# Kernel optimization log

Measured on AMD Instinct MI355X. Metric: run time of the kernel, lower is better.

## Reference

```python
import jax, jax.numpy as jnp
import numpy as np
from jax import lax

TAU = 2.0
NUM_HEADS = 8
EPS = 1e-5
ALPHA = 4.0  # surrogate sigmoid sharpness

@jax.custom_vjp
def heaviside(x):
    # torch.heaviside(x, 1.0): 1 for x >= 0 (value 1 at x==0), 0 for x < 0
    return (x >= 0).astype(x.dtype)

def _hv_fwd(x):
    return (x >= 0).astype(x.dtype), x

def _hv_bwd(x, g):
    s = jax.nn.sigmoid(x * ALPHA)
    return (g * s * (1.0 - s) * ALPHA,)

heaviside.defvjp(_hv_fwd, _hv_bwd)

def lif(x):
    # Leaky-integrate-fire recurrence over leading time axis. x: [T, ...]
    def step(v, xt):
        v = v + (xt - v) / TAU                 # leakage
        s = heaviside(v - 1.0)                 # fire (v_threshold = 1.0)
        v = (1.0 - lax.stop_gradient(s)) * v   # hard reset (detached spike)
        return v, s
    _, spikes = lax.scan(step, jnp.zeros_like(x[0]), x)
    return spikes

def conv1x1(x, w):
    # x: [T,B,Cin,H,W], w: [Cout,Cin] (1x1 conv, no bias)
    return jnp.einsum('tbchw,dc->tbdhw', x, w)

def bn(x, gamma, beta, mean, var):
    # BatchNorm2d in eval mode (running stats), per-channel over axis 2
    shp = (1, 1, -1, 1, 1)
    inv = gamma.reshape(shp) / jnp.sqrt(var.reshape(shp) + EPS)
    return (x - mean.reshape(shp)) * inv + beta.reshape(shp)

def setup_inputs():
    key = jax.random.key(0)
    ks = jax.random.split(key, 10)
    T, B, C, H, W = 4, 32, 256, 16, 16
    Cv = C  # lamda_ratio = 1

    def w_init(k, o, i):
        return jax.random.normal(k, (o, i), jnp.float32) * (1.0 / np.sqrt(i))

    def bn_params(k, c):
        k1, k2, k3, k4 = jax.random.split(k, 4)
        gamma = jax.random.uniform(k1, (c,), jnp.float32, 0.5, 1.5)
        beta = jax.random.normal(k2, (c,), jnp.float32) * 0.1
        mean = jax.random.normal(k3, (c,), jnp.float32) * 0.1
        var = jax.random.uniform(k4, (c,), jnp.float32, 0.5, 1.5)
        return gamma, beta, mean, var

    x = jax.random.normal(ks[0], (T, B, C, H, W), jnp.float32)
    q_w = w_init(ks[1], C, C)
    k_w = w_init(ks[2], C, C)
    v_w = w_init(ks[3], Cv, C)
    proj_w = w_init(ks[4], C, Cv)
    q_gamma, q_beta, q_mean, q_var = bn_params(ks[5], C)
    k_gamma, k_beta, k_mean, k_var = bn_params(ks[6], C)
    v_gamma, v_beta, v_mean, v_var = bn_params(ks[7], Cv)
    p_gamma, p_beta, p_mean, p_var = bn_params(ks[8], C)
    return {
        'x': x,
        'q_w': q_w, 'q_gamma': q_gamma, 'q_beta': q_beta, 'q_mean': q_mean, 'q_var': q_var,
        'k_w': k_w, 'k_gamma': k_gamma, 'k_beta': k_beta, 'k_mean': k_mean, 'k_var': k_var,
        'v_w': v_w, 'v_gamma': v_gamma, 'v_beta': v_beta, 'v_mean': v_mean, 'v_var': v_var,
        'proj_w': proj_w, 'p_gamma': p_gamma, 'p_beta': p_beta, 'p_mean': p_mean, 'p_var': p_var,
    }

def reference(x, q_w, q_gamma, q_beta, q_mean, q_var,
              k_w, k_gamma, k_beta, k_mean, k_var,
              v_w, v_gamma, v_beta, v_mean, v_var,
              proj_w, p_gamma, p_beta, p_mean, p_var):
    T, B, C, H, W = x.shape
    N = H * W
    Cv = v_w.shape[0]
    hd = C // NUM_HEADS
    hdv = Cv // NUM_HEADS
    scale = (C // NUM_HEADS) ** -0.5

    xs = lif(x)  # head_spike

    q = lif(bn(conv1x1(xs, q_w), q_gamma, q_beta, q_mean, q_var))  # [T,B,C,H,W] binary
    k = lif(bn(conv1x1(xs, k_w), k_gamma, k_beta, k_mean, k_var))
    v = lif(bn(conv1x1(xs, v_w), v_gamma, v_beta, v_mean, v_var))  # [T,B,Cv,H,W]

    # channel c = h*hd + d; flatten spatial -> tokens N, split heads
    q = q.reshape(T, B, NUM_HEADS, hd, N).transpose(0, 1, 2, 4, 3)   # [T,B,h,N,d]
    k = k.reshape(T, B, NUM_HEADS, hd, N).transpose(0, 1, 2, 4, 3)
    v = v.reshape(T, B, NUM_HEADS, hdv, N).transpose(0, 1, 2, 4, 3)  # [T,B,h,N,dv]

    attn = jnp.einsum('tbhnd,tbhmd->tbhnm', q, k)                    # QK^T
    out = jnp.einsum('tbhnm,tbhmd->tbhnd', attn, v) * (scale * 2.0)  # (QK^T)V * 2*scale

    out = out.transpose(0, 1, 2, 4, 3).reshape(T, B, Cv, N)          # [T,B,Cv,N]
    out = lif(out)                                                   # attn_spike
    out = out.reshape(T, B, Cv, H, W)
    out = bn(conv1x1(out, proj_w), p_gamma, p_beta, p_mean, p_var)   # [T,B,C,H,W]
    return out
```

## Files before the change

kernel.cpp:

```cpp
#include <hip/hip_runtime.h>

#define TT 4
#define BB 32
#define CC 256
#define NN 256
#define EPSf 1e-5f
#define MULTf 0.35355339059327373f
#define MARGINf 1e-3f
#define FLAG_CAP 524288u

typedef __attribute__((ext_vector_type(8))) short s16x8;
typedef __attribute__((ext_vector_type(4))) float f32x4;
typedef unsigned char uchar;
typedef unsigned int uint;
typedef unsigned short ushort;

__device__ __forceinline__ ushort f2bf_rn(float f) {
  uint u = __float_as_uint(f);
  u = (u + 0x7FFFu + ((u >> 16) & 1u)) >> 16;
  return (ushort)u;
}
__device__ __forceinline__ float bf2f(ushort b) {
  return __uint_as_float(((uint)b) << 16);
}

__device__ __forceinline__ void gload_lds16(const void* g, void* l) {
  __builtin_amdgcn_global_load_lds(
      (const __attribute__((address_space(1))) uint*)g,
      (__attribute__((address_space(3))) uint*)l, 16, 0, 0);
}

__global__ __launch_bounds__(256) void k_lif_frag(const float* __restrict__ x,
                                                  uchar* __restrict__ xsF,
                                                  uchar* __restrict__ xsP) {
#pragma clang fp contract(off)
  const int tid = threadIdx.x;
  const int nt = blockIdx.x;
  const int ks = blockIdx.y;
  const int b = blockIdx.z;
  const int nl = tid & 63;
  const int oct = tid >> 6;
  const int n = nt * 64 + nl;
  const int c0 = ks * 32 + oct * 8;
  const size_t stride = (size_t)BB * CC * NN;
  const float* xb = x + ((size_t)b * CC + c0) * NN + n;

  float v[8];
#pragma unroll
  for (int j = 0; j < 8; ++j) v[j] = 0.f;

#pragma unroll
  for (int t = 0; t < TT; ++t) {
    ushort sp[8];
    uint pm = 0;
#pragma unroll
    for (int j = 0; j < 8; ++j) {
      float xt = xb[t * stride + (size_t)j * NN];
      float d = (xt - v[j]) * 0.5f;
      v[j] = v[j] + d;
      bool s = (v[j] >= 1.0f);
      sp[j] = s ? (ushort)0x3F80 : (ushort)0;
      if (s) { v[j] = 0.f; pm |= 1u << j; }
    }
    uint4* dst = reinterpret_cast<uint4*>(xsF) +
                 (((size_t)(t * BB + b) * 16 + (n >> 4)) * 512 + ks * 64 + oct * 16 + (n & 15));
    uint4 o;
    o.x = (uint)sp[0] | ((uint)sp[1] << 16);
    o.y = (uint)sp[2] | ((uint)sp[3] << 16);
    o.z = (uint)sp[4] | ((uint)sp[5] << 16);
    o.w = (uint)sp[6] | ((uint)sp[7] << 16);
    *dst = o;
    xsP[(((size_t)(t * BB + b) * NN + n) << 5) + ks * 4 + oct] = (uchar)pm;
  }
}

__global__ __launch_bounds__(256) void k_prep_w(
    const float* __restrict__ qw, const float* __restrict__ kw,
    const float* __restrict__ vw, const float* __restrict__ pw,
    uchar* __restrict__ wfq, uchar* __restrict__ wfp) {
  const int gid = blockIdx.x * 256 + threadIdx.x;
  const int ob2 = gid >> 9;
  const int e = gid & 511;
  const int ks = e >> 6, l = e & 63;
  const float* W;
  uchar* outb;
  int ob_out, nob;
  if (ob2 < 48) {
    const int sel = ob2 >> 4;
    W = sel == 0 ? qw : (sel == 1 ? kw : vw);
    W += ((size_t)((ob2 & 15) * 16 + (l & 15))) * CC;
    outb = wfq; ob_out = ob2; nob = 48;
  } else {
    W = pw + ((size_t)((ob2 - 48) * 16 + (l & 15))) * CC;
    outb = wfp; ob_out = ob2 - 48; nob = 16;
  }
  const int c0 = ks * 32 + (l >> 4) * 8;
  float wv[8];
  *reinterpret_cast<float4*>(&wv[0]) = *reinterpret_cast<const float4*>(W + c0);
  *reinterpret_cast<float4*>(&wv[4]) = *reinterpret_cast<const float4*>(W + c0 + 4);
  ushort hi[8], lo[8];
#pragma unroll
  for (int j = 0; j < 8; ++j) {
    hi[j] = f2bf_rn(wv[j]);
    lo[j] = f2bf_rn(wv[j] - bf2f(hi[j]));
  }
  const size_t base = (((size_t)ob_out * 8 + ks) * 64 + l) * 16;
  const size_t sstr = (size_t)nob * 8 * 64 * 16;
  *reinterpret_cast<uint4*>(outb + base) = *reinterpret_cast<const uint4*>(hi);
  *reinterpret_cast<uint4*>(outb + sstr + base) = *reinterpret_cast<const uint4*>(lo);
}

__global__ __launch_bounds__(256, 2) void k_qkv_mfma(
    const uchar* __restrict__ xsF, const uchar* __restrict__ wfq,
    const float* __restrict__ qga, const float* __restrict__ qbe, const float* __restrict__ qme, const float* __restrict__ qva,
    const float* __restrict__ kga, const float* __restrict__ kbe, const float* __restrict__ kme, const float* __restrict__ kva,
    const float* __restrict__ vga, const float* __restrict__ vbe, const float* __restrict__ vme, const float* __restrict__ vva,
    ushort* __restrict__ qp, uint* __restrict__ flags) {
  __shared__ short lsB[4][8][64][8];
  const int tid = threadIdx.x;
  const int w = tid >> 6, lane = tid & 63;
  const int lhi = lane >> 4, llo = lane & 15;
  const int wr = w >> 1, wc = w & 1;
  const int oc0 = blockIdx.x * 64;
  const int ntile = blockIdx.y;
  const int b = blockIdx.z;
  const int sel = oc0 >> 8;
  const float* G  = sel == 0 ? qga : (sel == 1 ? kga : vga);
  const float* Be = sel == 0 ? qbe : (sel == 1 ? kbe : vbe);
  const float* Mn = sel == 0 ? qme : (sel == 1 ? kme : vme);
  const float* Vr = sel == 0 ? qva : (sel == 1 ? kva : vva);

  s16x8 wfr[2][2][8];
#pragma unroll
  for (int s = 0; s < 2; ++s)
#pragma unroll
    for (int mf = 0; mf < 2; ++mf) {
      const int ob = blockIdx.x * 4 + wr * 2 + mf;
#pragma unroll
      for (int ks = 0; ks < 8; ++ks)
        wfr[s][mf][ks] = *reinterpret_cast<const s16x8*>(
            wfq + ((((size_t)s * 48 + ob) * 8 + ks) * 64 + lane) * 16);
    }

  float inv8[2][4], mean8[2][4], beta8[2][4];
#pragma unroll
  for (int mf = 0; mf < 2; ++mf)
#pragma unroll
    for (int r = 0; r < 4; ++r) {
      const int ocb = (oc0 & 255) + wr * 32 + mf * 16 + lhi * 4 + r;
      inv8[mf][r] = G[ocb] / sqrtf(Vr[ocb] + EPSf);
      mean8[mf][r] = Mn[ocb];
      beta8[mf][r] = Be[ocb];
    }

  float vst[2][2][4];
#pragma unroll
  for (int mf = 0; mf < 2; ++mf)
#pragma unroll
    for (int nf = 0; nf < 2; ++nf)
#pragma unroll
      for (int r = 0; r < 4; ++r) vst[mf][nf][r] = 0.f;
  uint fl = 0;

  for (int t = 0; t < TT; ++t) {
    __syncthreads();
    const uchar* src = xsF + (((size_t)(t * BB + b) * 16 + ntile * 4) * 8192);
#pragma unroll
    for (int k2 = 0; k2 < 8; ++k2) {
      const int chunk = w * 8 + k2;
      gload_lds16(src + (size_t)chunk * 1024 + lane * 16,
                  reinterpret_cast<char*>(&lsB[0][0][0][0]) + chunk * 1024);
    }
    __syncthreads();

    f32x4 acc[2][2];
#pragma unroll
    for (int mf = 0; mf < 2; ++mf)
#pragma unroll
      for (int nf = 0; nf < 2; ++nf) acc[mf][nf] = (f32x4){0.f, 0.f, 0.f, 0.f};

#pragma unroll
    for (int ks = 0; ks < 8; ++ks) {
      s16x8 b0 = *reinterpret_cast<const s16x8*>(&lsB[wc * 2][ks][lane][0]);
      s16x8 b1 = *reinterpret_cast<const s16x8*>(&lsB[wc * 2 + 1][ks][lane][0]);
#pragma unroll
      for (int s = 0; s < 2; ++s)
#pragma unroll
        for (int mf = 0; mf < 2; ++mf) {
          acc[mf][0] = __builtin_amdgcn_mfma_f32_16x16x32_bf16(wfr[s][mf][ks], b0, acc[mf][0], 0, 0, 0);
          acc[mf][1] = __builtin_amdgcn_mfma_f32_16x16x32_bf16(wfr[s][mf][ks], b1, acc[mf][1], 0, 0, 0);
        }
    }

    ushort* qrow = qp + (size_t)(t * BB + b) * 768 * 16;
#pragma unroll
    for (int mf = 0; mf < 2; ++mf)
#pragma unroll
      for (int nf = 0; nf < 2; ++nf)
#pragma unroll
        for (int r = 0; r < 4; ++r) {
          float y = (acc[mf][nf][r] - mean8[mf][r]) * inv8[mf][r] + beta8[mf][r];
          float v = vst[mf][nf][r];
          v = v + (y - v) * 0.5f;
          const bool sp = (v >= 1.0f);
          if (fabsf(v - 1.0f) < MARGINf) fl |= 1u << ((mf * 2 + nf) * 4 + r);
          const unsigned long long m = __ballot(sp);
          if (llo == r) {
            const int oc = oc0 + wr * 32 + mf * 16 + lhi * 4 + r;
            const int nw = ntile * 4 + wc * 2 + nf;
            qrow[(size_t)oc * 16 + nw] = (ushort)((m >> (lhi * 16)) & 0xFFFFull);
          }
          vst[mf][nf][r] = sp ? 0.f : v;
        }
  }

  if (fl) {
    const int cnt = __popc(fl);
    uint base = atomicAdd(flags, (uint)cnt);
#pragma unroll
    for (int mf = 0; mf < 2; ++mf)
#pragma unroll
      for (int nf = 0; nf < 2; ++nf)
#pragma unroll
        for (int r = 0; r < 4; ++r)
          if (fl & (1u << ((mf * 2 + nf) * 4 + r))) {
            const int oc = oc0 + wr * 32 + mf * 16 + lhi * 4 + r;
            const int n = ntile * 64 + wc * 32 + nf * 16 + llo;
            if (base < FLAG_CAP) flags[4 + base] = (((uint)(b << 10) | (uint)oc) << 8) | (uint)n;
            base++;
          }
  }
}

__global__ __launch_bounds__(256) void k_fix(
    const uchar* __restrict__ xsP,
    const float* __restrict__ qw, const float* __restrict__ kw, const float* __restrict__ vw,
    const float* __restrict__ qga, const float* __restrict__ qbe, const float* __restrict__ qme, const float* __restrict__ qva,
    const float* __restrict__ kga, const float* __restrict__ kbe, const float* __restrict__ kme, const float* __restrict__ kva,
    const float* __restrict__ vga, const float* __restrict__ vbe, const float* __restrict__ vme, const float* __restrict__ vva,
    uint* __restrict__ qp32, const uint* __restrict__ flags) {
#pragma clang fp contract(off)
  const uint cnt = min(flags[0], FLAG_CAP);
  for (uint i = blockIdx.x * 256 + threadIdx.x; i < cnt; i += gridDim.x * 256) {
    const uint e = flags[4 + i];
    const int n = e & 255;
    const int oc = (e >> 8) & 1023;
    const int b = e >> 18;
    const int sel = oc >> 8, ocl = oc & 255;
    const float* W = (sel == 0 ? qw : (sel == 1 ? kw : vw)) + (size_t)ocl * CC;
    const float* G  = sel == 0 ? qga : (sel == 1 ? kga : vga);
    const float* Be = sel == 0 ? qbe : (sel == 1 ? kbe : vbe);
    const float* Mn = sel == 0 ? qme : (sel == 1 ? kme : vme);
    const float* Vr = sel == 0 ? qva : (sel == 1 ? kva : vva);

    uint bw[4][8];
#pragma unroll
    for (int t = 0; t < TT; ++t) {
      const uint4* p = reinterpret_cast<const uint4*>(
          xsP + (((size_t)(t * BB + b) * NN + n) << 5));
      uint4 a = p[0], c4 = p[1];
      bw[t][0] = a.x;  bw[t][1] = a.y;  bw[t][2] = a.z;  bw[t][3] = a.w;
      bw[t][4] = c4.x; bw[t][5] = c4.y; bw[t][6] = c4.z; bw[t][7] = c4.w;
    }

    const float4* W4 = reinterpret_cast<const float4*>(W);
    float a0 = 0.f, a1 = 0.f, a2 = 0.f, a3 = 0.f;
#pragma unroll
    for (int g = 0; g < 32; ++g) {
      const float4 w0 = W4[2 * g];
      const float4 w1 = W4[2 * g + 1];
      const uint s0 = bw[0][g >> 2] >> ((g & 3) * 8);
      const uint s1 = bw[1][g >> 2] >> ((g & 3) * 8);
      const uint s2 = bw[2][g >> 2] >> ((g & 3) * 8);
      const uint s3 = bw[3][g >> 2] >> ((g & 3) * 8);
      const float wv[8] = {w0.x, w0.y, w0.z, w0.w, w1.x, w1.y, w1.z, w1.w};
#pragma unroll
      for (int j = 0; j < 8; ++j) {
        a0 = fmaf(wv[j], (float)((s0 >> j) & 1u), a0);
        a1 = fmaf(wv[j], (float)((s1 >> j) & 1u), a1);
        a2 = fmaf(wv[j], (float)((s2 >> j) & 1u), a2);
        a3 = fmaf(wv[j], (float)((s3 >> j) & 1u), a3);
      }
    }
    float accs[4] = {a0, a1, a2, a3};

    const float inv = G[ocl] / sqrtf(Vr[ocl] + EPSf);
    const float mean = Mn[ocl], beta = Be[ocl];
    float v = 0.f;
#pragma unroll
    for (int t = 0; t < TT; ++t) {
      float xm = accs[t] - mean;
      float y = xm * inv;
      y = y + beta;
      float d = (y - v) * 0.5f;
      v = v + d;
      const bool sp = (v >= 1.0f);
      const size_t widx = ((size_t)(t * BB + b) * 768 + oc) * 8 + (n >> 5);
      const uint bit = 1u << (n & 31);
      if (sp) atomicOr(&qp32[widx], bit);
      else atomicAnd(&qp32[widx], ~bit);
      if (sp) v = 0.f;
    }
  }
}

__global__ __launch_bounds__(256) void k_attn(const ushort* __restrict__ qp,
                                              uchar* __restrict__ attnF) {
  __shared__ uint Qb[32][8], Kb[32][8], Vb[32][8];
  __shared__ int KtV[32][36];
  const int tid = threadIdx.x;
  const int b = blockIdx.x >> 3;
  const int h = blockIdx.x & 7;
  const int ch = tid >> 3, wv = tid & 7;
  const int n = tid;

  float vst[32];
#pragma unroll
  for (int j = 0; j < 32; ++j) vst[j] = 0.f;

  for (int t = 0; t < TT; ++t) {
    __syncthreads();
    const ushort* base = qp + (size_t)(t * BB + b) * 768 * 16;
    Qb[ch][wv] = *reinterpret_cast<const uint*>(base + (size_t)(h * 32 + ch) * 16 + wv * 2);
    Kb[ch][wv] = *reinterpret_cast<const uint*>(base + (size_t)(256 + h * 32 + ch) * 16 + wv * 2);
    Vb[ch][wv] = *reinterpret_cast<const uint*>(base + (size_t)(512 + h * 32 + ch) * 16 + wv * 2);
    __syncthreads();
#pragma unroll
    for (int p = 0; p < 4; ++p) {
      const int ee = tid + p * 256;
      const int ii = ee >> 5, jj = ee & 31;
      int s = 0;
#pragma unroll
      for (int ww = 0; ww < 8; ++ww) s += __popc(Kb[ii][ww] & Vb[jj][ww]);
      KtV[ii][jj] = s;
    }
    __syncthreads();
    int acc[32];
#pragma unroll
    for (int j = 0; j < 32; ++j) acc[j] = 0;
    for (int ii = 0; ii < 32; ++ii) {
      const uint qbit = (Qb[ii][n >> 5] >> (n & 31)) & 1u;
      if (qbit) {
        const int4* row = reinterpret_cast<const int4*>(&KtV[ii][0]);
#pragma unroll
        for (int j4 = 0; j4 < 8; ++j4) {
          int4 kk = row[j4];
          acc[j4 * 4 + 0] += kk.x;
          acc[j4 * 4 + 1] += kk.y;
          acc[j4 * 4 + 2] += kk.z;
          acc[j4 * 4 + 3] += kk.w;
        }
      }
    }
    uint smask = 0;
    {
#pragma clang fp contract(off)
#pragma unroll
      for (int j = 0; j < 32; ++j) {
        float y = (float)acc[j] * MULTf;
        float v = vst[j];
        float d = (y - v) * 0.5f;
        v = v + d;
        const bool sp = (v >= 1.0f);
        if (sp) smask |= 1u << j;
        vst[j] = sp ? 0.f : v;
      }
    }
    uint4* dst = reinterpret_cast<uint4*>(attnF) + (size_t)(t * BB + b) * 8192 + (n >> 4) * 512 + h * 64;
#pragma unroll
    for (int lhi = 0; lhi < 4; ++lhi) {
      uint wds[4];
#pragma unroll
      for (int p = 0; p < 4; ++p) {
        const uint b0 = (smask >> (lhi * 8 + p * 2)) & 1u;
        const uint b1 = (smask >> (lhi * 8 + p * 2 + 1)) & 1u;
        wds[p] = (b0 ? 0x3F80u : 0u) | (b1 ? 0x3F800000u : 0u);
      }
      uint4 o; o.x = wds[0]; o.y = wds[1]; o.z = wds[2]; o.w = wds[3];
      dst[lhi * 16 + (n & 15)] = o;
    }
  }
}

__global__ __launch_bounds__(256, 2) void k_proj_mfma(
    const uchar* __restrict__ attnF, const uchar* __restrict__ wfp,
    const float* __restrict__ pga, const float* __restrict__ pbe,
    const float* __restrict__ pme, const float* __restrict__ pva,
    float* __restrict__ out) {
  __shared__ short lsB[4][8][64][8];
  const int tid = threadIdx.x;
  const int w = tid >> 6, lane = tid & 63;
  const int lhi = lane >> 4, llo = lane & 15;
  const int wr = w >> 1, wc = w & 1;
  const int oc0 = blockIdx.x * 64;
  const int ntile = blockIdx.y;
  const int tb = blockIdx.z;

  s16x8 wfr[2][2][8];
#pragma unroll
  for (int s = 0; s < 2; ++s)
#pragma unroll
    for (int mf = 0; mf < 2; ++mf) {
      const int ob = blockIdx.x * 4 + wr * 2 + mf;
#pragma unroll
      for (int ks = 0; ks < 8; ++ks)
        wfr[s][mf][ks] = *reinterpret_cast<const s16x8*>(
            wfp + ((((size_t)s * 16 + ob) * 8 + ks) * 64 + lane) * 16);
    }

  float inv8[2][4], mean8[2][4], beta8[2][4];
#pragma unroll
  for (int mf = 0; mf < 2; ++mf)
#pragma unroll
    for (int r = 0; r < 4; ++r) {
      const int ocb = oc0 + wr * 32 + mf * 16 + lhi * 4 + r;
      inv8[mf][r] = pga[ocb] / sqrtf(pva[ocb] + EPSf);
      mean8[mf][r] = pme[ocb];
      beta8[mf][r] = pbe[ocb];
    }

  const uchar* src = attnF + (((size_t)tb * 16 + ntile * 4) * 8192);
#pragma unroll
  for (int k2 = 0; k2 < 8; ++k2) {
    const int chunk = w * 8 + k2;
    gload_lds16(src + (size_t)chunk * 1024 + lane * 16,
                reinterpret_cast<char*>(&lsB[0][0][0][0]) + chunk * 1024);
  }
  __syncthreads();

  f32x4 acc[2][2];
#pragma unroll
  for (int mf = 0; mf < 2; ++mf)
#pragma unroll
    for (int nf = 0; nf < 2; ++nf) acc[mf][nf] = (f32x4){0.f, 0.f, 0.f, 0.f};

#pragma unroll
  for (int ks = 0; ks < 8; ++ks) {
    s16x8 b0 = *reinterpret_cast<const s16x8*>(&lsB[wc * 2][ks][lane][0]);
    s16x8 b1 = *reinterpret_cast<const s16x8*>(&lsB[wc * 2 + 1][ks][lane][0]);
#pragma unroll
    for (int s = 0; s < 2; ++s)
#pragma unroll
      for (int mf = 0; mf < 2; ++mf) {
        acc[mf][0] = __builtin_amdgcn_mfma_f32_16x16x32_bf16(wfr[s][mf][ks], b0, acc[mf][0], 0, 0, 0);
        acc[mf][1] = __builtin_amdgcn_mfma_f32_16x16x32_bf16(wfr[s][mf][ks], b1, acc[mf][1], 0, 0, 0);
      }
  }

#pragma unroll
  for (int mf = 0; mf < 2; ++mf)
#pragma unroll
    for (int nf = 0; nf < 2; ++nf)
#pragma unroll
      for (int r = 0; r < 4; ++r) {
        const int oc = oc0 + wr * 32 + mf * 16 + lhi * 4 + r;
        const int nn = ntile * 64 + wc * 32 + nf * 16 + llo;
        float y = (acc[mf][nf][r] - mean8[mf][r]) * inv8[mf][r] + beta8[mf][r];
        out[((size_t)tb * CC + oc) * NN + nn] = y;
      }
}

extern "C" void kernel_launch(void* const* d_in, const int* in_sizes, int n_in,
                              void* d_out, int out_size, void* d_ws, size_t ws_size,
                              hipStream_t stream) {
  const float* x = (const float*)d_in[0];
  const float* q_w = (const float*)d_in[1];
  const float* q_g = (const float*)d_in[2];
  const float* q_b = (const float*)d_in[3];
  const float* q_m = (const float*)d_in[4];
  const float* q_v = (const float*)d_in[5];
  const float* k_w = (const float*)d_in[6];
  const float* k_g = (const float*)d_in[7];
  const float* k_b = (const float*)d_in[8];
  const float* k_m = (const float*)d_in[9];
  const float* k_v = (const float*)d_in[10];
  const float* v_w = (const float*)d_in[11];
  const float* v_g = (const float*)d_in[12];
  const float* v_b = (const float*)d_in[13];
  const float* v_m = (const float*)d_in[14];
  const float* v_v = (const float*)d_in[15];
  const float* p_w = (const float*)d_in[16];
  const float* p_g = (const float*)d_in[17];
  const float* p_b = (const float*)d_in[18];
  const float* p_m = (const float*)d_in[19];
  const float* p_v = (const float*)d_in[20];

  uchar* ws = (uchar*)d_ws;
  uchar* xsF  = ws;
  ushort* qp  = (ushort*)(ws + 16777216);
  uchar* wfq  = ws + 19922944;
  uchar* wfp  = ws + 20709376;
  uint* flags = (uint*)(ws + 20971520);
  uchar* xsP  = ws + 23068672;

  hipMemsetAsync(flags, 0, 16, stream);

  k_prep_w<<<dim3(128), 256, 0, stream>>>(q_w, k_w, v_w, p_w, wfq, wfp);
  k_lif_frag<<<dim3(4, 8, 32), 256, 0, stream>>>(x, xsF, xsP);
  k_qkv_mfma<<<dim3(12, 4, 32), 256, 0, stream>>>(xsF, wfq,
                                                  q_g, q_b, q_m, q_v,
                                                  k_g, k_b, k_m, k_v,
                                                  v_g, v_b, v_m, v_v,
                                                  qp, flags);
  k_fix<<<dim3(64), 256, 0, stream>>>(xsP, q_w, k_w, v_w,
                                      q_g, q_b, q_m, q_v,
                                      k_g, k_b, k_m, k_v,
                                      v_g, v_b, v_m, v_v,
                                      (uint*)qp, flags);
  k_attn<<<dim3(256), 256, 0, stream>>>(qp, xsF );
  k_proj_mfma<<<dim3(4, 4, 128), 256, 0, stream>>>(xsF, wfp, p_g, p_b, p_m, p_v,
                                                   (float*)d_out);
}
```

Before: 113.5 us.

## Double-buffer QKV staging, widen attention blocks, fold flag reset into prep kernel

The QKV MFMA kernel now double-buffers its shared-memory tile so the next timestep's load overlaps the current matmul. It also buffers spike masks in registers and writes them all after the loop. The attention kernel goes from 256 to 1024 threads per block, with each thread handling 8 output channels instead of 32 and doing one KtV element each, which lowers register pressure and raises parallelism. The separate memset of the flag counter is dropped and folded into the weight-prep kernel to save one launch. The costs are twice the LDS in the QKV kernel and larger blocks in the attention kernel, which may limit occupancy.

```diff
diff --git a/kernel.cpp b/kernel.cpp
--- a/kernel.cpp
+++ b/kernel.cpp
@@ -77,8 +77,10 @@
 __global__ __launch_bounds__(256) void k_prep_w(
     const float* __restrict__ qw, const float* __restrict__ kw,
     const float* __restrict__ vw, const float* __restrict__ pw,
-    uchar* __restrict__ wfq, uchar* __restrict__ wfp) {
+    uchar* __restrict__ wfq, uchar* __restrict__ wfp,
+    uint* __restrict__ flags) {
   const int gid = blockIdx.x * 256 + threadIdx.x;
+  if (gid < 4) flags[gid] = 0;
   const int ob2 = gid >> 9;
   const int e = gid & 511;
   const int ks = e >> 6, l = e & 63;
@@ -116,7 +118,7 @@
     const float* __restrict__ kga, const float* __restrict__ kbe, const float* __restrict__ kme, const float* __restrict__ kva,
     const float* __restrict__ vga, const float* __restrict__ vbe, const float* __restrict__ vme, const float* __restrict__ vva,
     ushort* __restrict__ qp, uint* __restrict__ flags) {
-  __shared__ short lsB[4][8][64][8];
+  __shared__ short lsB[2][4][8][64][8];
   const int tid = threadIdx.x;
   const int w = tid >> 6, lane = tid & 63;
   const int lhi = lane >> 4, llo = lane & 15;
@@ -153,25 +155,33 @@
       beta8[mf][r] = Be[ocb];
     }
 
-  float vst[2][2][4];
-#pragma unroll
-  for (int mf = 0; mf < 2; ++mf)
-#pragma unroll
-    for (int nf = 0; nf < 2; ++nf)
-#pragma unroll
-      for (int r = 0; r < 4; ++r) vst[mf][nf][r] = 0.f;
-  uint fl = 0;
-
-  for (int t = 0; t < TT; ++t) {
-    __syncthreads();
+  auto STAGE = [&](int buf, int t) {
     const uchar* src = xsF + (((size_t)(t * BB + b) * 16 + ntile * 4) * 8192);
 #pragma unroll
     for (int k2 = 0; k2 < 8; ++k2) {
       const int chunk = w * 8 + k2;
       gload_lds16(src + (size_t)chunk * 1024 + lane * 16,
-                  reinterpret_cast<char*>(&lsB[0][0][0][0]) + chunk * 1024);
-    }
-    __syncthreads();
+                  reinterpret_cast<char*>(&lsB[buf][0][0][0][0]) + chunk * 1024);
+    }
+  };
+
+  float vst[2][2][4];
+#pragma unroll
+  for (int mf = 0; mf < 2; ++mf)
+#pragma unroll
+    for (int nf = 0; nf < 2; ++nf)
+#pragma unroll
+      for (int r = 0; r < 4; ++r) vst[mf][nf][r] = 0.f;
+  uint fl = 0;
+  ushort qm[TT][4];
+
+  STAGE(0, 0);
+  __syncthreads();
+
+#pragma unroll
+  for (int t = 0; t < TT; ++t) {
+    const int cur = t & 1;
+    if (t + 1 < TT) STAGE(cur ^ 1, t + 1);
 
     f32x4 acc[2][2];
 #pragma unroll
@@ -181,8 +191,8 @@
 
 #pragma unroll
     for (int ks = 0; ks < 8; ++ks) {
-      s16x8 b0 = *reinterpret_cast<const s16x8*>(&lsB[wc * 2][ks][lane][0]);
-      s16x8 b1 = *reinterpret_cast<const s16x8*>(&lsB[wc * 2 + 1][ks][lane][0]);
+      s16x8 b0 = *reinterpret_cast<const s16x8*>(&lsB[cur][wc * 2][ks][lane][0]);
+      s16x8 b1 = *reinterpret_cast<const s16x8*>(&lsB[cur][wc * 2 + 1][ks][lane][0]);
 #pragma unroll
       for (int s = 0; s < 2; ++s)
 #pragma unroll
@@ -192,7 +202,6 @@
         }
     }
 
-    ushort* qrow = qp + (size_t)(t * BB + b) * 768 * 16;
 #pragma unroll
     for (int mf = 0; mf < 2; ++mf)
 #pragma unroll
@@ -205,13 +214,24 @@
           const bool sp = (v >= 1.0f);
           if (fabsf(v - 1.0f) < MARGINf) fl |= 1u << ((mf * 2 + nf) * 4 + r);
           const unsigned long long m = __ballot(sp);
-          if (llo == r) {
-            const int oc = oc0 + wr * 32 + mf * 16 + lhi * 4 + r;
-            const int nw = ntile * 4 + wc * 2 + nf;
-            qrow[(size_t)oc * 16 + nw] = (ushort)((m >> (lhi * 16)) & 0xFFFFull);
-          }
+          if (llo == r) qm[t][mf * 2 + nf] = (ushort)((m >> (lhi * 16)) & 0xFFFFull);
           vst[mf][nf][r] = sp ? 0.f : v;
         }
+    __syncthreads();
+  }
+
+  if (llo < 4) {
+#pragma unroll
+    for (int t = 0; t < TT; ++t) {
+      ushort* qrow = qp + (size_t)(t * BB + b) * 768 * 16;
+#pragma unroll
+      for (int mf = 0; mf < 2; ++mf)
+#pragma unroll
+        for (int nf = 0; nf < 2; ++nf) {
+          const int oc = oc0 + wr * 32 + mf * 16 + lhi * 4 + llo;
+          qrow[(size_t)oc * 16 + ntile * 4 + wc * 2 + nf] = qm[t][mf * 2 + nf];
+        }
+    }
   }
 
   if (fl) {
@@ -304,81 +324,77 @@
   }
 }
 
-__global__ __launch_bounds__(256) void k_attn(const ushort* __restrict__ qp,
-                                              uchar* __restrict__ attnF) {
+__global__ __launch_bounds__(1024) void k_attn(const ushort* __restrict__ qp,
+                                               uchar* __restrict__ attnF) {
   __shared__ uint Qb[32][8], Kb[32][8], Vb[32][8];
-  __shared__ int KtV[32][36];
+  __shared__ int KtV[32][32];
   const int tid = threadIdx.x;
   const int b = blockIdx.x >> 3;
   const int h = blockIdx.x & 7;
-  const int ch = tid >> 3, wv = tid & 7;
-  const int n = tid;
-
-  float vst[32];
-#pragma unroll
-  for (int j = 0; j < 32; ++j) vst[j] = 0.f;
+  const int n = tid & 255;
+  const int jg = tid >> 8;
+  const int wordn = n >> 5, bitn = n & 31;
+
+  float vst[8];
+#pragma unroll
+  for (int j = 0; j < 8; ++j) vst[j] = 0.f;
 
   for (int t = 0; t < TT; ++t) {
     __syncthreads();
     const ushort* base = qp + (size_t)(t * BB + b) * 768 * 16;
-    Qb[ch][wv] = *reinterpret_cast<const uint*>(base + (size_t)(h * 32 + ch) * 16 + wv * 2);
-    Kb[ch][wv] = *reinterpret_cast<const uint*>(base + (size_t)(256 + h * 32 + ch) * 16 + wv * 2);
-    Vb[ch][wv] = *reinterpret_cast<const uint*>(base + (size_t)(512 + h * 32 + ch) * 16 + wv * 2);
+    if (tid < 768) {
+      const int arr = tid >> 8;
+      const int idx = tid & 255;
+      const int ch = idx >> 3, wv2 = idx & 7;
+      const uint val = *reinterpret_cast<const uint*>(
+          base + (size_t)(arr * 256 + h * 32 + ch) * 16 + wv2 * 2);
+      uint(*dst)[8] = (arr == 0) ? Qb : (arr == 1) ? Kb : Vb;
+      dst[ch][wv2] = val;
+    }
     __syncthreads();
-#pragma unroll
-    for (int p = 0; p < 4; ++p) {
-      const int ee = tid + p * 256;
-      const int ii = ee >> 5, jj = ee & 31;
+    {
+      const int ii = tid >> 5, jj = tid & 31;
       int s = 0;
 #pragma unroll
-      for (int ww = 0; ww < 8; ++ww) s += __popc(Kb[ii][ww] & Vb[jj][ww]);
+      for (int w8 = 0; w8 < 8; ++w8) s += __popc(Kb[ii][w8] & Vb[jj][w8]);
       KtV[ii][jj] = s;
     }
     __syncthreads();
-    int acc[32];
-#pragma unroll
-    for (int j = 0; j < 32; ++j) acc[j] = 0;
+    int acc[8];
+#pragma unroll
+    for (int j = 0; j < 8; ++j) acc[j] = 0;
+#pragma unroll 4
     for (int ii = 0; ii < 32; ++ii) {
-      const uint qbit = (Qb[ii][n >> 5] >> (n & 31)) & 1u;
-      if (qbit) {
-        const int4* row = reinterpret_cast<const int4*>(&KtV[ii][0]);
-#pragma unroll
-        for (int j4 = 0; j4 < 8; ++j4) {
-          int4 kk = row[j4];
-          acc[j4 * 4 + 0] += kk.x;
-          acc[j4 * 4 + 1] += kk.y;
-          acc[j4 * 4 + 2] += kk.z;
-          acc[j4 * 4 + 3] += kk.w;
-        }
-      }
-    }
-    uint smask = 0;
+      const int qb = (int)((Qb[ii][wordn] >> bitn) & 1u);
+      const int4 k0 = *reinterpret_cast<const int4*>(&KtV[ii][jg * 8]);
+      const int4 k1 = *reinterpret_cast<const int4*>(&KtV[ii][jg * 8 + 4]);
+      acc[0] += k0.x * qb; acc[1] += k0.y * qb;
+      acc[2] += k0.z * qb; acc[3] += k0.w * qb;
+      acc[4] += k1.x * qb; acc[5] += k1.y * qb;
+      acc[6] += k1.z * qb; acc[7] += k1.w * qb;
+    }
+    ushort sbit[8];
     {
 #pragma clang fp contract(off)
 #pragma unroll
-      for (int j = 0; j < 32; ++j) {
+      for (int j = 0; j < 8; ++j) {
         float y = (float)acc[j] * MULTf;
         float v = vst[j];
         float d = (y - v) * 0.5f;
         v = v + d;
         const bool sp = (v >= 1.0f);
-        if (sp) smask |= 1u << j;
+        sbit[j] = sp ? (ushort)0x3F80 : (ushort)0;
         vst[j] = sp ? 0.f : v;
       }
     }
-    uint4* dst = reinterpret_cast<uint4*>(attnF) + (size_t)(t * BB + b) * 8192 + (n >> 4) * 512 + h * 64;
-#pragma unroll
-    for (int lhi = 0; lhi < 4; ++lhi) {
-      uint wds[4];
-#pragma unroll
-      for (int p = 0; p < 4; ++p) {
-        const uint b0 = (smask >> (lhi * 8 + p * 2)) & 1u;
-        const uint b1 = (smask >> (lhi * 8 + p * 2 + 1)) & 1u;
-        wds[p] = (b0 ? 0x3F80u : 0u) | (b1 ? 0x3F800000u : 0u);
-      }
-      uint4 o; o.x = wds[0]; o.y = wds[1]; o.z = wds[2]; o.w = wds[3];
-      dst[lhi * 16 + (n & 15)] = o;
-    }
+    uint4 o;
+    o.x = (uint)sbit[0] | ((uint)sbit[1] << 16);
+    o.y = (uint)sbit[2] | ((uint)sbit[3] << 16);
+    o.z = (uint)sbit[4] | ((uint)sbit[5] << 16);
+    o.w = (uint)sbit[6] | ((uint)sbit[7] << 16);
+    uint4* dst4 = reinterpret_cast<uint4*>(attnF) +
+                  (((size_t)(t * BB + b) * 16 + (n >> 4)) * 512 + h * 64 + jg * 16 + (n & 15));
+    *dst4 = o;
   }
 }
 
@@ -493,9 +509,7 @@
   uint* flags = (uint*)(ws + 20971520);
   uchar* xsP  = ws + 23068672;
 
-  hipMemsetAsync(flags, 0, 16, stream);
-
-  k_prep_w<<<dim3(128), 256, 0, stream>>>(q_w, k_w, v_w, p_w, wfq, wfp);
+  k_prep_w<<<dim3(128), 256, 0, stream>>>(q_w, k_w, v_w, p_w, wfq, wfp, flags);
   k_lif_frag<<<dim3(4, 8, 32), 256, 0, stream>>>(x, xsF, xsP);
   k_qkv_mfma<<<dim3(12, 4, 32), 256, 0, stream>>>(xsF, wfq,
                                                   q_g, q_b, q_m, q_v,
@@ -507,7 +521,7 @@
                                       k_g, k_b, k_m, k_v,
                                       v_g, v_b, v_m, v_v,
                                       (uint*)qp, flags);
-  k_attn<<<dim3(256), 256, 0, stream>>>(qp, xsF );
+  k_attn<<<dim3(256), 1024, 0, stream>>>(qp, xsF );
   k_proj_mfma<<<dim3(4, 4, 128), 256, 0, stream>>>(xsF, wfp, p_g, p_b, p_m, p_v,
                                                    (float*)d_out);
 }
```

Result: no change. 114.1 us (+0.5%).
